# Optimization experiments

Measured on AMD Instinct MI355X. Metric: run time of the kernel, lower is better.

## Reference

```python
import jax, jax.numpy as jnp
import numpy as np

B, H, K, L, V = 4096, 1024, 10, 64, 80  # batch, hidden, mixtures, char_len, vocab

def setup_inputs() -> dict:
    key = jax.random.key(0)
    k1, k2, k3, k4 = jax.random.split(key, 4)
    return {
        "x": jax.random.normal(k1, (B, H), dtype=jnp.float32),
        "chars": jax.random.normal(k2, (B, L, V), dtype=jnp.float32),
        "W": jax.random.normal(k3, (H, 3 * K), dtype=jnp.float32) * 0.02,
        "b": jax.random.normal(k4, (3 * K,), dtype=jnp.float32) * 0.02,
    }

def reference(x, chars, W, b):
    # Linear: [B, 3K]
    out = x @ W + b
    alpha_raw, beta_raw, kappa_raw = jnp.split(out, 3, axis=1)  # each [B, K]
    alpha = jnp.exp(alpha_raw)[:, :, None]            # [B, K, 1]
    beta = jnp.exp(beta_raw)[:, :, None]              # [B, K, 1]
    # kappa_prev is zero on first call -> kappa = exp(kappa_raw)
    kappa = jnp.exp(kappa_raw)[:, :, None]            # [B, K, 1]
    u = jnp.arange(L, dtype=jnp.float32)[None, None, :]  # [1, 1, L]
    phi = jnp.sum(alpha * jnp.exp(-beta * (kappa - u) ** 2), axis=1)  # [B, L]
    window = jnp.einsum('bl,blv->bv', phi, chars)     # [B, V]
    return window
```

## Files before the change

### kernel.cpp

```cpp
#include <hip/hip_runtime.h>
#include <math.h>

constexpr int Bn = 4096;
constexpr int Hn = 1024;
constexpr int Kn = 10;
constexpr int Ln = 64;
constexpr int Vn = 80;
constexpr int NJ = 3 * Kn;
constexpr int R  = 4;
constexpr int NT = 256;

__global__ __launch_bounds__(NT, 6) void window_kernel(
    const float* __restrict__ x,
    const float* __restrict__ chars,
    const float* __restrict__ W,
    const float* __restrict__ bias,
    float* __restrict__ out)
{
    __shared__ __align__(16) char smem_u[R * Hn * 4];
    float4* xs4   = (float4*)smem_u;
    float4* cpart = (float4*)smem_u;

    __shared__ float part[R * 256];
    __shared__ float abk[R * NJ];
    __shared__ float phi_s[R * Ln];

    const int t    = threadIdx.x;
    const int row0 = blockIdx.x * R;

    const float4* x4 = (const float4*)x;
#pragma unroll
    for (int r = 0; r < R; ++r)
        xs4[r * (Hn / 4) + t] = x4[(size_t)(row0 + r) * (Hn / 4) + t];
    __syncthreads();

    const int j = t & 31;
    const int g = t >> 5;
    float acc0 = 0.f, acc1 = 0.f, acc2 = 0.f, acc3 = 0.f;
    if (j < NJ) {
        const float* Wp = W + j;
        const int h0 = g * 128;
#pragma unroll 4
        for (int ii = 0; ii < 128; ii += 4) {
            const int h  = h0 + ii;
            const int h4 = h >> 2;
            float4 xa = xs4[0 * (Hn / 4) + h4];
            float4 xb = xs4[1 * (Hn / 4) + h4];
            float4 xc = xs4[2 * (Hn / 4) + h4];
            float4 xd = xs4[3 * (Hn / 4) + h4];
            float w0 = Wp[(h + 0) * NJ];
            float w1 = Wp[(h + 1) * NJ];
            float w2 = Wp[(h + 2) * NJ];
            float w3 = Wp[(h + 3) * NJ];
            acc0 += w0 * xa.x + w1 * xa.y + w2 * xa.z + w3 * xa.w;
            acc1 += w0 * xb.x + w1 * xb.y + w2 * xb.z + w3 * xb.w;
            acc2 += w0 * xc.x + w1 * xc.y + w2 * xc.z + w3 * xc.w;
            acc3 += w0 * xd.x + w1 * xd.y + w2 * xd.z + w3 * xd.w;
        }
    }
    part[0 * 256 + g * 32 + j] = acc0;
    part[1 * 256 + g * 32 + j] = acc1;
    part[2 * 256 + g * 32 + j] = acc2;
    part[3 * 256 + g * 32 + j] = acc3;
    __syncthreads();

    if (t < R * NJ) {
        const int r = t / NJ, jj = t % NJ;
        float s = bias[jj];
#pragma unroll
        for (int gg = 0; gg < 8; ++gg) s += part[r * 256 + gg * 32 + jj];
        abk[r * NJ + jj] = __expf(s);
    }
    __syncthreads();

    {
        const int r = t >> 6, l = t & 63;
        const float lf = (float)l;
        const float* ab = abk + r * NJ;
        float ph = 0.f;
#pragma unroll
        for (int k = 0; k < Kn; ++k) {
            float a  = ab[k];
            float bt = ab[Kn + k];
            float kp = ab[2 * Kn + k];
            float d  = kp - lf;
            ph += a * __expf(-bt * d * d);
        }
        phi_s[r * Ln + l] = ph;
    }
    __syncthreads();

    const float4* c4 = (const float4*)chars;
    if (t < 240) {
        const int v4  = t % 20;
        const int g12 = t / 20;
        float4 s0 = make_float4(0.f, 0.f, 0.f, 0.f);
        float4 s1 = s0, s2 = s0, s3 = s0;
        for (int l = g12; l < Ln; l += 12) {
            const int off = l * 20 + v4;
            float4 cA = c4[(size_t)(row0 + 0) * 1280 + off];
            float4 cB = c4[(size_t)(row0 + 1) * 1280 + off];
            float4 cC = c4[(size_t)(row0 + 2) * 1280 + off];
            float4 cD = c4[(size_t)(row0 + 3) * 1280 + off];
            float p0 = phi_s[0 * Ln + l];
            float p1 = phi_s[1 * Ln + l];
            float p2 = phi_s[2 * Ln + l];
            float p3 = phi_s[3 * Ln + l];
            s0.x += p0 * cA.x; s0.y += p0 * cA.y; s0.z += p0 * cA.z; s0.w += p0 * cA.w;
            s1.x += p1 * cB.x; s1.y += p1 * cB.y; s1.z += p1 * cB.z; s1.w += p1 * cB.w;
            s2.x += p2 * cC.x; s2.y += p2 * cC.y; s2.z += p2 * cC.z; s2.w += p2 * cC.w;
            s3.x += p3 * cD.x; s3.y += p3 * cD.y; s3.z += p3 * cD.z; s3.w += p3 * cD.w;
        }
        cpart[(0 * 12 + g12) * 20 + v4] = s0;
        cpart[(1 * 12 + g12) * 20 + v4] = s1;
        cpart[(2 * 12 + g12) * 20 + v4] = s2;
        cpart[(3 * 12 + g12) * 20 + v4] = s3;
    }
    __syncthreads();

    if (t < 80) {
        const int r  = t / 20;
        const int vv = t % 20;
        float4 s = make_float4(0.f, 0.f, 0.f, 0.f);
#pragma unroll
        for (int gg = 0; gg < 12; ++gg) {
            float4 p = cpart[(r * 12 + gg) * 20 + vv];
            s.x += p.x; s.y += p.y; s.z += p.z; s.w += p.w;
        }
        ((float4*)out)[(size_t)(row0 + r) * 20 + vv] = s;
    }
}

extern "C" void kernel_launch(void* const* d_in, const int* in_sizes, int n_in,
                              void* d_out, int out_size, void* d_ws, size_t ws_size,
                              hipStream_t stream) {
    const float* x     = (const float*)d_in[0];
    const float* chars = (const float*)d_in[1];
    const float* W     = (const float*)d_in[2];
    const float* bias  = (const float*)d_in[3];
    float* out = (float*)d_out;

    window_kernel<<<Bn / R, NT, 0, stream>>>(x, chars, W, bias, out);
}
```

Baseline: 153.3 us.

## Split fused kernel into phi computation and chars reduction kernels

Breaks the single fused kernel into two launches: one computes the linear layer, the exps and phi into a workspace buffer, and a second kernel streams chars with one thread per row/vocab float4 across all 64 positions. This drops the cross-group partial reduction through shared memory and lets each stage pick its own block shape and occupancy. The cost is an extra kernel launch, a phi round trip through global memory, and idle lanes (12 of 32 per row) in the window kernel. It also raises the unroll factor of the matvec loop.

```diff
diff --git a/kernel.cpp b/kernel.cpp
--- a/kernel.cpp
+++ b/kernel.cpp
@@ -7,30 +7,26 @@
 constexpr int Ln = 64;
 constexpr int Vn = 80;
 constexpr int NJ = 3 * Kn;
-constexpr int R  = 4;
-constexpr int NT = 256;
+constexpr int RA = 4;
+constexpr int RB = 8;
 
-__global__ __launch_bounds__(NT, 6) void window_kernel(
+__global__ __launch_bounds__(256) void phi_kernel(
     const float* __restrict__ x,
-    const float* __restrict__ chars,
     const float* __restrict__ W,
     const float* __restrict__ bias,
-    float* __restrict__ out)
+    float* __restrict__ phi)
 {
-    __shared__ __align__(16) char smem_u[R * Hn * 4];
-    float4* xs4   = (float4*)smem_u;
-    float4* cpart = (float4*)smem_u;
+    __shared__ __align__(16) float xs[RA * Hn];
+    __shared__ float part[RA * 256];
+    __shared__ float abk[RA * NJ];
 
-    __shared__ float part[R * 256];
-    __shared__ float abk[R * NJ];
-    __shared__ float phi_s[R * Ln];
-
+    float4* xs4 = (float4*)xs;
     const int t    = threadIdx.x;
-    const int row0 = blockIdx.x * R;
+    const int row0 = blockIdx.x * RA;
 
     const float4* x4 = (const float4*)x;
 #pragma unroll
-    for (int r = 0; r < R; ++r)
+    for (int r = 0; r < RA; ++r)
         xs4[r * (Hn / 4) + t] = x4[(size_t)(row0 + r) * (Hn / 4) + t];
     __syncthreads();
 
@@ -40,7 +36,7 @@
     if (j < NJ) {
         const float* Wp = W + j;
         const int h0 = g * 128;
-#pragma unroll 4
+#pragma unroll 8
         for (int ii = 0; ii < 128; ii += 4) {
             const int h  = h0 + ii;
             const int h4 = h >> 2;
@@ -64,7 +60,7 @@
     part[3 * 256 + g * 32 + j] = acc3;
     __syncthreads();
 
-    if (t < R * NJ) {
+    if (t < RA * NJ) {
         const int r = t / NJ, jj = t % NJ;
         float s = bias[jj];
 #pragma unroll
@@ -86,48 +82,38 @@
             float d  = kp - lf;
             ph += a * __expf(-bt * d * d);
         }
-        phi_s[r * Ln + l] = ph;
+        phi[(size_t)row0 * Ln + t] = ph;
     }
+}
+
+__global__ __launch_bounds__(256) void window_kernel(
+    const float* __restrict__ chars,
+    const float* __restrict__ phi,
+    float* __restrict__ out)
+{
+    __shared__ float phis[RB * Ln];
+
+    const int t    = threadIdx.x;
+    const int row0 = blockIdx.x * RB;
+
+    phis[t]       = phi[(size_t)row0 * Ln + t];
+    phis[t + 256] = phi[(size_t)row0 * Ln + t + 256];
     __syncthreads();
 
-    const float4* c4 = (const float4*)chars;
-    if (t < 240) {
-        const int v4  = t % 20;
-        const int g12 = t / 20;
-        float4 s0 = make_float4(0.f, 0.f, 0.f, 0.f);
-        float4 s1 = s0, s2 = s0, s3 = s0;
-        for (int l = g12; l < Ln; l += 12) {
-            const int off = l * 20 + v4;
-            float4 cA = c4[(size_t)(row0 + 0) * 1280 + off];
-            float4 cB = c4[(size_t)(row0 + 1) * 1280 + off];
-            float4 cC = c4[(size_t)(row0 + 2) * 1280 + off];
-            float4 cD = c4[(size_t)(row0 + 3) * 1280 + off];
-            float p0 = phi_s[0 * Ln + l];
-            float p1 = phi_s[1 * Ln + l];
-            float p2 = phi_s[2 * Ln + l];
-            float p3 = phi_s[3 * Ln + l];
-            s0.x += p0 * cA.x; s0.y += p0 * cA.y; s0.z += p0 * cA.z; s0.w += p0 * cA.w;
-            s1.x += p1 * cB.x; s1.y += p1 * cB.y; s1.z += p1 * cB.z; s1.w += p1 * cB.w;
-            s2.x += p2 * cC.x; s2.y += p2 * cC.y; s2.z += p2 * cC.z; s2.w += p2 * cC.w;
-            s3.x += p3 * cD.x; s3.y += p3 * cD.y; s3.z += p3 * cD.z; s3.w += p3 * cD.w;
+    const int v4 = t & 31;
+    const int r  = t >> 5;
+    if (v4 < 20) {
+        const int b = row0 + r;
+        const float4* c4 = (const float4*)chars + (size_t)b * (Ln * Vn / 4) + v4;
+        const float* ph = phis + r * Ln;
+        float4 acc = make_float4(0.f, 0.f, 0.f, 0.f);
+#pragma unroll 16
+        for (int l = 0; l < Ln; ++l) {
+            float4 c = c4[(size_t)l * (Vn / 4)];
+            float  p = ph[l];
+            acc.x += p * c.x; acc.y += p * c.y; acc.z += p * c.z; acc.w += p * c.w;
         }
-        cpart[(0 * 12 + g12) * 20 + v4] = s0;
-        cpart[(1 * 12 + g12) * 20 + v4] = s1;
-        cpart[(2 * 12 + g12) * 20 + v4] = s2;
-        cpart[(3 * 12 + g12) * 20 + v4] = s3;
-    }
-    __syncthreads();
-
-    if (t < 80) {
-        const int r  = t / 20;
-        const int vv = t % 20;
-        float4 s = make_float4(0.f, 0.f, 0.f, 0.f);
-#pragma unroll
-        for (int gg = 0; gg < 12; ++gg) {
-            float4 p = cpart[(r * 12 + gg) * 20 + vv];
-            s.x += p.x; s.y += p.y; s.z += p.z; s.w += p.w;
-        }
-        ((float4*)out)[(size_t)(row0 + r) * 20 + vv] = s;
+        ((float4*)out)[(size_t)b * (Vn / 4) + v4] = acc;
     }
 }
 
@@ -139,6 +125,8 @@
     const float* W     = (const float*)d_in[2];
     const float* bias  = (const float*)d_in[3];
     float* out = (float*)d_out;
+    float* phi = (float*)d_ws;
 
-    window_kernel<<<Bn / R, NT, 0, stream>>>(x, chars, W, bias, out);
+    phi_kernel<<<Bn / RA, 256, 0, stream>>>(x, W, bias, phi);
+    window_kernel<<<Bn / RB, 256, 0, stream>>>(chars, phi, out);
 }
```

Result: faster. 148.6 us (-3.1%).
